# Optimization experiments

Hardware: AMD Instinct MI355X
Metric: run time of the kernel (lower is better)

Reference implementation:

```python
import jax, jax.numpy as jnp
import numpy as np

B, G = 32, 100                      # batch, max ground-truth boxes per image
LEVELS = [(80, 8), (40, 16), (20, 32)]  # (grid_size, stride) for 640x640 input -> 8400 anchors
NUM_CLASSES = 1


def _grids():
    xs, ys, ss = [], [], []
    for n, s in LEVELS:
        yy, xx = np.meshgrid(np.arange(n), np.arange(n), indexing="ij")
        xs.append(xx.reshape(-1)); ys.append(yy.reshape(-1)); ss.append(np.full(n * n, s))
    f = lambda a: jnp.asarray(np.concatenate(a), jnp.float32)[None]
    return f(xs), f(ys), f(ss)


def setup_inputs() -> dict:
    key = jax.random.key(0)
    k1, k2, k3, k4, k5, k6 = jax.random.split(key, 6)
    x_shifts, y_shifts, strides = _grids()
    A = x_shifts.shape[1]
    # decoded predictions: cx,cy in image, positive w,h; obj/cls are raw logits
    cxy = jax.random.uniform(k1, (B, A, 2), minval=0.0, maxval=640.0)
    wh = jax.random.uniform(k2, (B, A, 2), minval=4.0, maxval=128.0)
    objcls = jax.random.normal(k3, (B, A, 1 + NUM_CLASSES))
    outputs = jnp.concatenate([cxy, wh, objcls], -1)
    # labels: (class, cx, cy, w, h), zero-padded past the per-image gt count
    gxy = jax.random.uniform(k4, (B, G, 2), minval=32.0, maxval=608.0)
    gwh = jax.random.uniform(k5, (B, G, 2), minval=8.0, maxval=128.0)
    ngt = jax.random.randint(k6, (B,), 1, G + 1)
    valid = (jnp.arange(G)[None, :] < ngt[:, None]).astype(jnp.float32)[..., None]
    labels = jnp.concatenate([jnp.zeros((B, G, 1)), gxy, gwh], -1) * valid
    return {"outputs": outputs, "labels": labels, "x_shifts": x_shifts,
            "y_shifts": y_shifts, "expanded_strides": strides}


def _pairwise_iou_cxcywh(a, b):  # a [G,4] gt, b [A,4] preds -> [G,A]
    tl = jnp.maximum(a[:, None, :2] - a[:, None, 2:] / 2, b[None, :, :2] - b[None, :, 2:] / 2)
    br = jnp.minimum(a[:, None, :2] + a[:, None, 2:] / 2, b[None, :, :2] + b[None, :, 2:] / 2)
    inter = jnp.prod(jnp.maximum(br - tl, 0.0), -1)
    area_a = jnp.prod(a[:, 2:], -1)[:, None]
    area_b = jnp.prod(b[:, 2:], -1)[None, :]
    return inter / (area_a + area_b - inter + 1e-12)


def _assign_one(out, lab, xc, yc, st):
    """SimOTA assignment for one image. out [A,6], lab [G,5], xc/yc/st [A]."""
    bbox, obj, cls = out[:, :4], out[:, 4:5], out[:, 5:]
    valid_gt = lab.sum(-1) > 0                       # [G] mirrors nlabel logic
    gt = lab[:, 1:5]
    gt_cls = lab[:, 0].astype(jnp.int32)
    gcx, gcy, gw, gh = gt[:, 0:1], gt[:, 1:2], gt[:, 2:3], gt[:, 3:4]
    # anchor center inside gt box
    in_box = ((xc[None] > gcx - gw / 2) & (xc[None] < gcx + gw / 2) &
              (yc[None] > gcy - gh / 2) & (yc[None] < gcy + gh / 2))
    # anchor center within 2.5*stride of gt center
    r = 2.5 * st[None]
    in_ctr = (jnp.abs(xc[None] - gcx) < r) & (jnp.abs(yc[None] - gcy) < r)
    in_box &= valid_gt[:, None]
    in_ctr &= valid_gt[:, None]
    fg = (in_box | in_ctr).any(0)                    # [A] candidate fg anchors
    geo = in_box & in_ctr                            # [G,A]
    pair_ok = fg[None, :] & valid_gt[:, None]
    ious = _pairwise_iou_cxcywh(gt, bbox)            # [G,A]
    iou_m = jnp.where(pair_ok, ious, 0.0)
    # cls cost: BCE( sqrt(sigmoid(cls)*sigmoid(obj)), one_hot(gt_cls) )
    p = jnp.sqrt(jax.nn.sigmoid(cls) * jax.nn.sigmoid(obj))      # [A,C]
    t = jax.nn.one_hot(gt_cls, NUM_CLASSES)                       # [G,C]
    cls_cost = -(t[:, None, :] * jnp.log(p[None] + 1e-9) +
                 (1.0 - t[:, None, :]) * jnp.log(1.0 - p[None] + 1e-9)).sum(-1)
    cost = cls_cost + 3.0 * (-jnp.log(ious + 1e-8)) + 1e5 * (~geo)
    cost = jnp.where(pair_ok, cost, 1e9)             # exclude non-fg / padded gts
    # dynamic-k: k_g = clamp(sum(top-10 ious), min 1)
    topk_ious = jax.lax.top_k(iou_m, 10)[0]
    dyn_k = jnp.maximum(topk_ious.sum(-1).astype(jnp.int32), 1)  # [G]
    # rank anchors per gt by ascending cost; pick rank < dyn_k
    ranks = jnp.argsort(jnp.argsort(cost, axis=1), axis=1)
    matching = (ranks < dyn_k[:, None]) & pair_ok
    # resolve anchors matched to >1 gt: keep the min-cost gt
    cnt = matching.sum(0)
    best_gt = jnp.argmin(cost, 0)                    # [A]
    matching = jnp.where((cnt > 1)[None, :], jnp.arange(G)[:, None] == best_gt[None, :], matching)
    fg_final = matching.any(0)                       # [A]
    pred_iou = (matching.astype(ious.dtype) * ious).sum(0)       # [A]
    matched_gt = jnp.argmax(matching, 0)             # [A]
    cls_t = jax.nn.one_hot(gt_cls[matched_gt], NUM_CLASSES) * pred_iou[:, None]
    cls_t = jnp.where(fg_final[:, None], cls_t, 0.0)
    return fg_final, cls_t


def reference(outputs, labels, x_shifts, y_shifts, expanded_strides):
    st = expanded_strides[0]
    xc = (x_shifts[0] + 0.5) * st
    yc = (y_shifts[0] + 0.5) * st
    fg, cls_t = jax.vmap(lambda o, l: _assign_one(o, l, xc, yc, st))(outputs, labels)
    # assignment runs under no_grad in the original
    fg = jax.lax.stop_gradient(fg)
    cls_t = jax.lax.stop_gradient(cls_t)
    logits = outputs[:, :, 5:]                       # [B,A,C]
    bce = cls_t * jax.nn.softplus(-logits) + (1.0 - cls_t) * jax.nn.softplus(logits)
    num_fg = jnp.maximum(fg.sum().astype(jnp.float32), 1.0)
    return (bce * fg[..., None]).sum() / num_fg
```

## Files before the change

### kernel.cpp

```cpp
#include <hip/hip_runtime.h>
#include <hip/hip_bf16.h>
#include <stdint.h>

#define BB 32
#define GG 100
#define AA 8400
#define TPB 256
#define NCH 33
#define TKB 512
#define BA (BB*AA)
#define NG (BB*GG)
#define NB2 (BB*GG)
#define NITB 17
#define PCAP 8416
#define GCAP 128
#define SCAP (GG*10)

typedef __hip_bfloat16 bf16;

struct P {
  const void *outs, *labs, *ss;
  float4 *box4, *gtb, *gtc;
  float2 *aux2;
  float *pcc, *zl;
  int   *sel_a;
  float *sel_iou;
  int   *cnt, *own;
  float *pb, *pf;
  int *gmax;
  float *out;
};

__device__ __forceinline__ int dtypeFlag(const void* ss){
  return (((const uint32_t*)ss)[0] == 0x41000000u) ? 1 : 0;
}
__device__ __forceinline__ float ld(const void* p, int i, int isf32){
  return isf32 ? ((const float*)p)[i] : __bfloat162float(((const bf16*)p)[i]);
}
__device__ __forceinline__ void ageom(int a, float& xc, float& yc, float& r){
  int x, y, s;
  if (a < 6400){ x = a % 80; y = a / 80; s = 8; }
  else if (a < 8000){ int q = a - 6400; x = q % 40; y = q / 40; s = 16; }
  else { int q = a - 8000; x = q % 20; y = q / 20; s = 32; }
  float fs = (float)s;
  xc = ((float)x + 0.5f) * fs;
  yc = ((float)y + 0.5f) * fs;
  r  = 2.5f * fs;
}
__device__ __forceinline__ uint32_t apack2(int a){
  int x, y, s, lvl;
  if (a < 6400){ x = a % 80; y = a / 80; s = 8; lvl = 0; }
  else if (a < 8000){ int q = a - 6400; x = q % 40; y = q / 40; s = 16; lvl = 1; }
  else { int q = a - 8000; x = q % 20; y = q / 20; s = 32; lvl = 2; }
  return (uint32_t)(x*s + s/2) | ((uint32_t)(y*s + s/2) << 10) | ((uint32_t)lvl << 20);
}

__global__ __launch_bounds__(TPB) void kA(P p){
  __shared__ float4 s_gtb[GG], s_gtc[GG];
  __shared__ float s_o[TPB*6];
  __shared__ int s_ng;
  int t = threadIdx.x;
  int c = blockIdx.x, b = blockIdx.y;
  int isf = dtypeFlag(p.ss);
  if (t == 0) s_ng = 0;
  {
    int s = c*TPB + t;
    if (s < SCAP) p.sel_a[b*SCAP + s] = -1;
  }
  int nel = min(TPB*6, AA*6 - c*(TPB*6));
  if (isf){
    const float4* src = (const float4*)((const float*)p.outs + (size_t)b*AA*6 + (size_t)c*(TPB*6));
    float4* dst = (float4*)s_o;
    for (int i = t; i < nel/4; i += TPB) dst[i] = src[i];
  } else {
    const uint4* src = (const uint4*)((const bf16*)p.outs + (size_t)b*AA*6 + (size_t)c*(TPB*6));
    for (int i = t; i < nel/8; i += TPB){
      uint4 u = src[i];
      int o = i*8;
      s_o[o+0]=__uint_as_float(u.x<<16); s_o[o+1]=__uint_as_float(u.x&0xffff0000u);
      s_o[o+2]=__uint_as_float(u.y<<16); s_o[o+3]=__uint_as_float(u.y&0xffff0000u);
      s_o[o+4]=__uint_as_float(u.z<<16); s_o[o+5]=__uint_as_float(u.z&0xffff0000u);
      s_o[o+6]=__uint_as_float(u.w<<16); s_o[o+7]=__uint_as_float(u.w&0xffff0000u);
    }
  }
  __syncthreads();
  if (t < GG){
    int i = b*GG + t;
    float l0 = ld(p.labs, i*5  , isf);
    float gcx= ld(p.labs, i*5+1, isf);
    float gcy= ld(p.labs, i*5+2, isf);
    float gw = ld(p.labs, i*5+3, isf);
    float gh = ld(p.labs, i*5+4, isf);
    int valid = (l0+gcx+gcy+gw+gh) > 0.f;
    float4 vb = make_float4(gcx-gw*0.5f, gcy-gh*0.5f, gcx+gw*0.5f, gcy+gh*0.5f);
    float4 vc = make_float4(gcx, gcy, gw*gh, valid ? 1.f : 0.f);
    s_gtb[t] = vb; s_gtc[t] = vc;
    if (c == 0){ p.gtb[i] = vb; p.gtc[i] = vc; }
    if (valid) atomicMax(&s_ng, t+1);
  }
  __syncthreads();
  int ng = s_ng;
  if (c == 0 && t == 0) p.gmax[b] = ng;
  int a = c*TPB + t;
  if (a < AA){
    float cx=s_o[t*6], cy=s_o[t*6+1], w=s_o[t*6+2], h=s_o[t*6+3], ob=s_o[t*6+4], cl=s_o[t*6+5];
    int idx = b*AA + a;
    p.box4[idx] = make_float4(cx-w*0.5f, cy-h*0.5f, cx+w*0.5f, cy+h*0.5f);
    float so = 1.f/(1.f+expf(-ob));
    float sc = 1.f/(1.f+expf(-cl));
    float pccv = -logf(sqrtf(sc*so) + 1e-9f);
    float xc, yc, r; ageom(a, xc, yc, r);
    int fg = 0;
    for (int g = 0; g < ng; ++g){
      float4 gb = s_gtb[g], gc = s_gtc[g];
      bool inb = (xc>gb.x)&&(xc<gb.z)&&(yc>gb.y)&&(yc<gb.w);
      bool inc = (fabsf(xc-gc.x)<r)&&(fabsf(yc-gc.y)<r);
      fg |= (gc.w != 0.f) && (inb||inc);
    }
    float area = w*h;
    p.aux2[idx] = make_float2(fg ? area : -area, __uint_as_float(apack2(a)));
    p.pcc[idx] = pccv;
    p.zl [idx] = cl;
    p.cnt[idx] = 0;
    p.own[idx] = 0x7fffffff;
  }
}

__global__ __launch_bounds__(TKB) void kB(P p){
  __shared__ float s_pos[PCAP];
  __shared__ float s_gcost[GCAP];
  __shared__ int   s_gpos[GCAP];
  __shared__ int   s_pcnt, s_gcnt;
  int t = threadIdx.x;
  int lane = t & 63, wid = t >> 6;
  int item = blockIdx.x;
  int b = item / GG, g = item - b*GG;
  if (t == 0){ s_pcnt = 0; s_gcnt = 0; }
  float4 gc = p.gtc[b*GG+g];
  if (gc.w == 0.f) return;
  float4 gb = p.gtb[b*GG+g];
  float glx=gb.x, gly=gb.y, ghx=gb.z, ghy=gb.w, gcx=gc.x, gcy=gc.y, ga=gc.z;
  int base = b*AA;
  unsigned long long lmlt = (1ull<<lane) - 1ull;
  __syncthreads();

  for (int it = 0; it < NITB; ++it){
    int pos = it*TKB + t;
    bool ovl = false, geo = false;
    float v = 0.f, cst = 0.f;
    if (pos < AA){
      float2 aux = p.aux2[base+pos];
      float4 bx  = p.box4[base+pos];
      bool fg = aux.x > 0.f;
      uint32_t u = __float_as_uint(aux.y);
      float xc = (float)(u & 1023u), yc = (float)((u>>10)&1023u);
      float r  = (float)(20u << (u>>20));
      bool inb = (xc>glx)&&(xc<ghx)&&(yc>gly)&&(yc<ghy);
      geo = inb && (fabsf(xc-gcx)<r) && (fabsf(yc-gcy)<r);
      float tlx=fmaxf(glx,bx.x), tly=fmaxf(gly,bx.y);
      float brx=fminf(ghx,bx.z), bry=fminf(ghy,bx.w);
      float iw=brx-tlx, ih=bry-tly;
      ovl = fg && (iw>0.f) && (ih>0.f);
      if (ovl | geo){
        float area = fabsf(aux.x);
        float inter = fmaxf(iw,0.f)*fmaxf(ih,0.f);
        v = inter/(ga + area - inter + 1e-12f);
        if (geo) cst = p.pcc[base+pos] + 3.f*(-logf(v+1e-8f));
      }
    }
    unsigned long long m1 = __ballot(ovl);
    if (m1){
      int ldr = (int)(__ffsll(m1)-1);
      int off;
      if (lane == ldr) off = atomicAdd(&s_pcnt, __popcll(m1));
      off = __shfl(off, ldr);
      if (ovl) s_pos[off + __popcll(m1 & lmlt)] = v;
    }
    unsigned long long m2 = __ballot(geo);
    if (m2){
      int ldr = (int)(__ffsll(m2)-1);
      int off;
      if (lane == ldr) off = atomicAdd(&s_gcnt, __popcll(m2));
      off = __shfl(off, ldr);
      if (geo){
        int q = off + __popcll(m2 & lmlt);
        s_gcost[q] = cst; s_gpos[q] = pos;
      }
    }
  }
  __syncthreads();
  if (wid) return;

  int pcnt = s_pcnt, gcnt = s_gcnt;

  float lmax = -1.f;
  for (int i = lane; i < pcnt; i += 64) lmax = fmaxf(lmax, s_pos[i]);
  float sum = 0.f;
  for (int k = 0; k < 10; ++k){
    float gv = lmax;
#pragma unroll
    for (int off=32; off; off>>=1) gv = fmaxf(gv, __shfl_xor(gv, off));
    if (gv <= 0.f) break;
    sum += gv;
    unsigned long long ms = __ballot(lmax == gv);
    if ((int)(__ffsll(ms)-1) == lane){
      bool fnd = false; float nl = -1.f;
      for (int i = lane; i < pcnt; i += 64){
        float vv = s_pos[i];
        if (!fnd && vv == gv){ fnd = true; vv = -1.f; s_pos[i] = vv; }
        nl = fmaxf(nl, vv);
      }
      lmax = nl;
    }
  }
  int dk = (int)sum; if (dk<1) dk=1; if (dk>10) dk=10;

  float c0=3.0e38f, c1=3.0e38f; int p0=0x7fffffff, p1=0x7fffffff;
  if (lane < gcnt){ c0 = s_gcost[lane]; p0 = s_gpos[lane]; }
  if (lane+64 < gcnt){ c1 = s_gcost[lane+64]; p1 = s_gpos[lane+64]; }
  if (c1 < c0 || (c1==c0 && p1<p0)){
    float tc=c0; c0=c1; c1=tc; int tp=p0; p0=p1; p1=tp;
  }
  int mysel = -1, take = 0;
  for (int k = 0; k < dk; ++k){
    float gv=c0; int gi=p0;
#pragma unroll
    for (int off=32; off; off>>=1){
      float ov=__shfl_xor(gv,off); int oi=__shfl_xor(gi,off);
      if (ov<gv || (ov==gv && oi<gi)){ gv=ov; gi=oi; }
    }
    if (gv >= 2.9e38f) break;
    if (lane == k) mysel = gi;
    take++;
    if (c0==gv && p0==gi){ c0=c1; p0=p1; c1=3.0e38f; p1=0x7fffffff; }
  }

  float lastc = -3.0e38f; int lastp = -1;
  for (int k = take; k < dk; ++k){
    float bc = 3.0e38f; int bp = 0x7fffffff;
    int n64 = (AA + 63) >> 6;
    for (int it = 0; it < n64; ++it){
      int pos = (it<<6) + lane;
      if (pos < AA){
        float2 aux = p.aux2[base+pos];
        bool fg = aux.x > 0.f;
        if (fg){
          uint32_t u = __float_as_uint(aux.y);
          float xc = (float)(u & 1023u), yc = (float)((u>>10)&1023u);
          float r  = (float)(20u << (u>>20));
          bool inb = (xc>glx)&&(xc<ghx)&&(yc>gly)&&(yc<ghy);
          bool geo2 = inb && (fabsf(xc-gcx)<r) && (fabsf(yc-gcy)<r);
          if (!geo2){
            float4 bx = p.box4[base+pos];
            float tlx=fmaxf(glx,bx.x), tly=fmaxf(gly,bx.y);
            float brx=fminf(ghx,bx.z), bry=fminf(ghy,bx.w);
            float iw=fmaxf(brx-tlx,0.f), ih=fmaxf(bry-tly,0.f);
            float inter=iw*ih;
            float area = fabsf(aux.x);
            float v = inter/(ga + area - inter + 1e-12f);
            float cst = p.pcc[base+pos] + 3.f*(-logf(v+1e-8f)) + 100000.f;
            bool gt = (cst > lastc) || (cst == lastc && pos > lastp);
            bool lt = (cst < bc)   || (cst == bc   && pos < bp);
            if (gt && lt){ bc = cst; bp = pos; }
          }
        }
      }
    }
#pragma unroll
    for (int off=32; off; off>>=1){
      float ov=__shfl_xor(bc,off); int oi=__shfl_xor(bp,off);
      if (ov<bc || (ov==bc && oi<bp)){ bc=ov; bp=oi; }
    }
    if (bc >= 2.9e38f) break;
    if (lane == k) mysel = bp;
    lastc = bc; lastp = bp;
  }

  if (mysel >= 0){
    int a = mysel;
    float4 bx = p.box4[base+a];
    float area = fabsf(p.aux2[base+a].x);
    float tlx=fmaxf(glx,bx.x), tly=fmaxf(gly,bx.y);
    float brx=fminf(ghx,bx.z), bry=fminf(ghy,bx.w);
    float iw=fmaxf(brx-tlx,0.f), ih=fmaxf(bry-tly,0.f);
    float inter=iw*ih;
    float iou=inter/(ga + area - inter + 1e-12f);
    int slot = g*10 + lane;
    p.sel_a [b*SCAP + slot] = a;
    p.sel_iou[b*SCAP + slot] = iou;
    atomicAdd(&p.cnt[base+a], 1);
    atomicMin(&p.own[base+a], slot);
  }
}

__global__ __launch_bounds__(64) void kR(P p){
  int lane = threadIdx.x;
  int item = blockIdx.x;
  int b = item / GG, g = item - b*GG;
  int base = b*AA;
  int a = -1, cgt = 0;
  bool ownr = false;
  float iouv = 0.f;
  if (lane < 10){
    int slot = g*10 + lane;
    a = p.sel_a[b*SCAP + slot];
    if (a >= 0 && p.own[base+a] == slot){
      ownr = true;
      cgt = p.cnt[base+a];
      iouv = p.sel_iou[b*SCAP + slot];
    }
  }
  unsigned long long cm = __ballot(ownr && cgt > 1);
  if (cm){
    int ng = p.gmax[b];
    while (cm){
      int s = (int)(__ffsll(cm)-1); cm &= cm - 1ull;
      int aa = __shfl(a, s);
      float area = fabsf(p.aux2[base+aa].x);
      float pccv = p.pcc[base+aa];
      float4 bx = p.box4[base+aa];
      float xc,yc,r; ageom(aa,xc,yc,r);
      float bc = 3.9e38f, bi = 0.f; int bg = 0x7fffffff;
      for (int g2 = lane; g2 < ng; g2 += 64){
        float4 gbb = p.gtb[b*GG+g2], gcc = p.gtc[b*GG+g2];
        float cost, iou2 = 0.f;
        if (gcc.w != 0.f){
          float tlx=fmaxf(gbb.x,bx.x), tly=fmaxf(gbb.y,bx.y);
          float brx=fminf(gbb.z,bx.z), bry=fminf(gbb.w,bx.w);
          float iw=fmaxf(brx-tlx,0.f), ih=fmaxf(bry-tly,0.f);
          float inter=iw*ih;
          iou2 = inter/(gcc.z + area - inter + 1e-12f);
          bool inb=(xc>gbb.x)&&(xc<gbb.z)&&(yc>gbb.y)&&(yc<gbb.w);
          bool inc=(fabsf(xc-gcc.x)<r)&&(fabsf(yc-gcc.y)<r);
          cost = pccv + 3.f*(-logf(iou2+1e-8f)) + ((inb&&inc)?0.f:100000.f);
        } else cost = 1e9f;
        if (cost < bc){ bc=cost; bi=iou2; bg=g2; }
      }
#pragma unroll
      for (int off=32; off; off>>=1){
        float oc=__shfl_xor(bc,off), oi=__shfl_xor(bi,off);
        int og=__shfl_xor(bg,off);
        if (oc<bc || (oc==bc && og<bg)){ bc=oc; bi=oi; bg=og; }
      }
      if (lane == s) iouv = bi;
    }
  }
  float bce = 0.f, fgv = 0.f;
  if (lane < 10 && ownr){
    float z = p.zl[base+a];
    float e = expf(-fabsf(z));
    float spz = fmaxf(z,0.f)+log1pf(e);
    float spn = fmaxf(-z,0.f)+log1pf(e);
    bce = iouv*spn + (1.f-iouv)*spz;
    fgv = 1.f;
  }
#pragma unroll
  for (int off=32; off; off>>=1){
    bce += __shfl_xor(bce, off);
    fgv += __shfl_xor(fgv, off);
  }
  if (lane == 0){ p.pb[item] = bce; p.pf[item] = fgv; }
}

__global__ __launch_bounds__(TPB) void kD(P p){
  int t = threadIdx.x;
  float sb=0.f, sf=0.f;
  for (int i = t; i < NB2; i += TPB){ sb += p.pb[i]; sf += p.pf[i]; }
#pragma unroll
  for (int off=32; off; off>>=1){
    sb += __shfl_xor(sb, off);
    sf += __shfl_xor(sf, off);
  }
  __shared__ float s_b[4], s_f[4];
  int lane = t & 63, wid = t >> 6;
  if (lane==0){ s_b[wid]=sb; s_f[wid]=sf; }
  __syncthreads();
  if (t==0){
    float tb=s_b[0]+s_b[1]+s_b[2]+s_b[3];
    float tf=s_f[0]+s_f[1]+s_f[2]+s_f[3];
    p.out[0] = tb / fmaxf(tf, 1.f);
  }
}

extern "C" void kernel_launch(void* const* d_in, const int* in_sizes, int n_in,
                              void* d_out, int out_size, void* d_ws, size_t ws_size,
                              hipStream_t stream) {
  P p;
  p.outs = d_in[0];
  p.labs = d_in[1];
  p.ss   = d_in[4];
  char* w = (char*)d_ws;
  p.box4  = (float4*)w; w += (size_t)BA*sizeof(float4);
  p.gtb   = (float4*)w; w += (size_t)NG*sizeof(float4);
  p.gtc   = (float4*)w; w += (size_t)NG*sizeof(float4);
  p.aux2  = (float2*)w; w += (size_t)BA*sizeof(float2);
  p.pcc   = (float*)w;  w += (size_t)BA*sizeof(float);
  p.zl    = (float*)w;  w += (size_t)BA*sizeof(float);
  p.sel_a = (int*)w;    w += (size_t)BB*SCAP*sizeof(int);
  p.sel_iou=(float*)w;  w += (size_t)BB*SCAP*sizeof(float);
  p.cnt   = (int*)w;    w += (size_t)BA*sizeof(int);
  p.own   = (int*)w;    w += (size_t)BA*sizeof(int);
  p.gmax  = (int*)w;    w += (size_t)BB*sizeof(int);
  p.pb    = (float*)w;  w += (size_t)NB2*sizeof(float);
  p.pf    = (float*)w;  w += (size_t)NB2*sizeof(float);
  p.out   = (float*)d_out;

  kA<<<dim3(NCH, BB), TPB, 0, stream>>>(p);
  kB<<<BB*GG, TKB, 0, stream>>>(p);
  kR<<<NB2, 64, 0, stream>>>(p);
  kD<<<1, TPB, 0, stream>>>(p);
}
```

Before: 151.3 us.

## Drop precomputed per-anchor buffers; pack anchor metadata and read raw outputs

kA no longer writes box4, aux2, pcc and zl per anchor. It writes only a packed 32-bit word holding anchor geometry plus the fg flag, and the per-anchor count and owner are merged into one int2. kB and kR now read the raw prediction rows directly and recompute box corners, area and pair cost on the fly. The fg loop also exits early once a match is found. This is meant to cut workspace write and read traffic, at the cost of repeated transcendental work and strided 24-byte row reads in the per-GT blocks.

```diff
diff --git a/kernel.cpp b/kernel.cpp
--- a/kernel.cpp
+++ b/kernel.cpp
@@ -20,12 +20,11 @@
 
 struct P {
   const void *outs, *labs, *ss;
-  float4 *box4, *gtb, *gtc;
-  float2 *aux2;
-  float *pcc, *zl;
+  float4 *gtb, *gtc;
+  uint32_t *pk;
+  int2  *cnow;
   int   *sel_a;
   float *sel_iou;
-  int   *cnt, *own;
   float *pb, *pf;
   int *gmax;
   float *out;
@@ -36,6 +35,36 @@
 }
 __device__ __forceinline__ float ld(const void* p, int i, int isf32){
   return isf32 ? ((const float*)p)[i] : __bfloat162float(((const bf16*)p)[i]);
+}
+__device__ __forceinline__ void ldbox(const void* outs, int isf, size_t row,
+                                      float& cx, float& cy, float& w, float& h){
+  if (isf){
+    const float2* rw = (const float2*)((const float*)outs + row*6);
+    float2 r01 = rw[0], r23 = rw[1];
+    cx=r01.x; cy=r01.y; w=r23.x; h=r23.y;
+  } else {
+    const uint32_t* rw = (const uint32_t*)((const bf16*)outs + row*6);
+    uint32_t w0 = rw[0], w1 = rw[1];
+    cx=__uint_as_float(w0<<16); cy=__uint_as_float(w0&0xffff0000u);
+    w =__uint_as_float(w1<<16); h =__uint_as_float(w1&0xffff0000u);
+  }
+}
+__device__ __forceinline__ void ldoc(const void* outs, int isf, size_t row,
+                                     float& ob, float& cl){
+  if (isf){
+    const float2* rw = (const float2*)((const float*)outs + row*6);
+    float2 r45 = rw[2];
+    ob=r45.x; cl=r45.y;
+  } else {
+    const uint32_t* rw = (const uint32_t*)((const bf16*)outs + row*6);
+    uint32_t w2 = rw[2];
+    ob=__uint_as_float(w2<<16); cl=__uint_as_float(w2&0xffff0000u);
+  }
+}
+__device__ __forceinline__ float pccf(float ob, float cl){
+  float so = 1.f/(1.f+expf(-ob));
+  float sc = 1.f/(1.f+expf(-cl));
+  return -logf(sqrtf(sc*so) + 1e-9f);
 }
 __device__ __forceinline__ void ageom(int a, float& xc, float& yc, float& r){
   int x, y, s;
@@ -57,7 +86,6 @@
 
 __global__ __launch_bounds__(TPB) void kA(P p){
   __shared__ float4 s_gtb[GG], s_gtc[GG];
-  __shared__ float s_o[TPB*6];
   __shared__ int s_ng;
   int t = threadIdx.x;
   int c = blockIdx.x, b = blockIdx.y;
@@ -66,22 +94,6 @@
   {
     int s = c*TPB + t;
     if (s < SCAP) p.sel_a[b*SCAP + s] = -1;
-  }
-  int nel = min(TPB*6, AA*6 - c*(TPB*6));
-  if (isf){
-    const float4* src = (const float4*)((const float*)p.outs + (size_t)b*AA*6 + (size_t)c*(TPB*6));
-    float4* dst = (float4*)s_o;
-    for (int i = t; i < nel/4; i += TPB) dst[i] = src[i];
-  } else {
-    const uint4* src = (const uint4*)((const bf16*)p.outs + (size_t)b*AA*6 + (size_t)c*(TPB*6));
-    for (int i = t; i < nel/8; i += TPB){
-      uint4 u = src[i];
-      int o = i*8;
-      s_o[o+0]=__uint_as_float(u.x<<16); s_o[o+1]=__uint_as_float(u.x&0xffff0000u);
-      s_o[o+2]=__uint_as_float(u.y<<16); s_o[o+3]=__uint_as_float(u.y&0xffff0000u);
-      s_o[o+4]=__uint_as_float(u.z<<16); s_o[o+5]=__uint_as_float(u.z&0xffff0000u);
-      s_o[o+6]=__uint_as_float(u.w<<16); s_o[o+7]=__uint_as_float(u.w&0xffff0000u);
-    }
   }
   __syncthreads();
   if (t < GG){
@@ -103,12 +115,7 @@
   if (c == 0 && t == 0) p.gmax[b] = ng;
   int a = c*TPB + t;
   if (a < AA){
-    float cx=s_o[t*6], cy=s_o[t*6+1], w=s_o[t*6+2], h=s_o[t*6+3], ob=s_o[t*6+4], cl=s_o[t*6+5];
     int idx = b*AA + a;
-    p.box4[idx] = make_float4(cx-w*0.5f, cy-h*0.5f, cx+w*0.5f, cy+h*0.5f);
-    float so = 1.f/(1.f+expf(-ob));
-    float sc = 1.f/(1.f+expf(-cl));
-    float pccv = -logf(sqrtf(sc*so) + 1e-9f);
     float xc, yc, r; ageom(a, xc, yc, r);
     int fg = 0;
     for (int g = 0; g < ng; ++g){
@@ -116,13 +123,10 @@
       bool inb = (xc>gb.x)&&(xc<gb.z)&&(yc>gb.y)&&(yc<gb.w);
       bool inc = (fabsf(xc-gc.x)<r)&&(fabsf(yc-gc.y)<r);
       fg |= (gc.w != 0.f) && (inb||inc);
-    }
-    float area = w*h;
-    p.aux2[idx] = make_float2(fg ? area : -area, __uint_as_float(apack2(a)));
-    p.pcc[idx] = pccv;
-    p.zl [idx] = cl;
-    p.cnt[idx] = 0;
-    p.own[idx] = 0x7fffffff;
+      if (fg) break;
+    }
+    p.pk[idx]   = apack2(a) | (fg ? 0x80000000u : 0u);
+    p.cnow[idx] = make_int2(0, 0x7fffffff);
   }
 }
 
@@ -141,6 +145,7 @@
   float4 gb = p.gtb[b*GG+g];
   float glx=gb.x, gly=gb.y, ghx=gb.z, ghy=gb.w, gcx=gc.x, gcy=gc.y, ga=gc.z;
   int base = b*AA;
+  int isf = dtypeFlag(p.ss);
   unsigned long long lmlt = (1ull<<lane) - 1ull;
   __syncthreads();
 
@@ -149,23 +154,26 @@
     bool ovl = false, geo = false;
     float v = 0.f, cst = 0.f;
     if (pos < AA){
-      float2 aux = p.aux2[base+pos];
-      float4 bx  = p.box4[base+pos];
-      bool fg = aux.x > 0.f;
-      uint32_t u = __float_as_uint(aux.y);
+      uint32_t u = p.pk[base+pos];
+      bool fg = (u & 0x80000000u) != 0;
       float xc = (float)(u & 1023u), yc = (float)((u>>10)&1023u);
-      float r  = (float)(20u << (u>>20));
+      float r  = (float)(20u << ((u>>20)&3u));
       bool inb = (xc>glx)&&(xc<ghx)&&(yc>gly)&&(yc<ghy);
       geo = inb && (fabsf(xc-gcx)<r) && (fabsf(yc-gcy)<r);
-      float tlx=fmaxf(glx,bx.x), tly=fmaxf(gly,bx.y);
-      float brx=fminf(ghx,bx.z), bry=fminf(ghy,bx.w);
+      float cx,cy,w,h; ldbox(p.outs, isf, (size_t)(base+pos), cx,cy,w,h);
+      float blx=cx-w*0.5f, bly=cy-h*0.5f, bhx=cx+w*0.5f, bhy=cy+h*0.5f;
+      float tlx=fmaxf(glx,blx), tly=fmaxf(gly,bly);
+      float brx=fminf(ghx,bhx), bry=fminf(ghy,bhy);
       float iw=brx-tlx, ih=bry-tly;
       ovl = fg && (iw>0.f) && (ih>0.f);
       if (ovl | geo){
-        float area = fabsf(aux.x);
+        float area = w*h;
         float inter = fmaxf(iw,0.f)*fmaxf(ih,0.f);
         v = inter/(ga + area - inter + 1e-12f);
-        if (geo) cst = p.pcc[base+pos] + 3.f*(-logf(v+1e-8f));
+        if (geo){
+          float ob,cl; ldoc(p.outs, isf, (size_t)(base+pos), ob, cl);
+          cst = pccf(ob,cl) + 3.f*(-logf(v+1e-8f));
+        }
       }
     }
     unsigned long long m1 = __ballot(ovl);
@@ -242,23 +250,24 @@
     for (int it = 0; it < n64; ++it){
       int pos = (it<<6) + lane;
       if (pos < AA){
-        float2 aux = p.aux2[base+pos];
-        bool fg = aux.x > 0.f;
+        uint32_t u = p.pk[base+pos];
+        bool fg = (u & 0x80000000u) != 0;
         if (fg){
-          uint32_t u = __float_as_uint(aux.y);
           float xc = (float)(u & 1023u), yc = (float)((u>>10)&1023u);
-          float r  = (float)(20u << (u>>20));
+          float r  = (float)(20u << ((u>>20)&3u));
           bool inb = (xc>glx)&&(xc<ghx)&&(yc>gly)&&(yc<ghy);
           bool geo2 = inb && (fabsf(xc-gcx)<r) && (fabsf(yc-gcy)<r);
           if (!geo2){
-            float4 bx = p.box4[base+pos];
-            float tlx=fmaxf(glx,bx.x), tly=fmaxf(gly,bx.y);
-            float brx=fminf(ghx,bx.z), bry=fminf(ghy,bx.w);
+            float cx,cy,w,h; ldbox(p.outs, isf, (size_t)(base+pos), cx,cy,w,h);
+            float blx=cx-w*0.5f, bly=cy-h*0.5f, bhx=cx+w*0.5f, bhy=cy+h*0.5f;
+            float tlx=fmaxf(glx,blx), tly=fmaxf(gly,bly);
+            float brx=fminf(ghx,bhx), bry=fminf(ghy,bhy);
             float iw=fmaxf(brx-tlx,0.f), ih=fmaxf(bry-tly,0.f);
             float inter=iw*ih;
-            float area = fabsf(aux.x);
+            float area = w*h;
             float v = inter/(ga + area - inter + 1e-12f);
-            float cst = p.pcc[base+pos] + 3.f*(-logf(v+1e-8f)) + 100000.f;
+            float ob,cl; ldoc(p.outs, isf, (size_t)(base+pos), ob, cl);
+            float cst = pccf(ob,cl) + 3.f*(-logf(v+1e-8f)) + 100000.f;
             bool gt = (cst > lastc) || (cst == lastc && pos > lastp);
             bool lt = (cst < bc)   || (cst == bc   && pos < bp);
             if (gt && lt){ bc = cst; bp = pos; }
@@ -278,18 +287,19 @@
 
   if (mysel >= 0){
     int a = mysel;
-    float4 bx = p.box4[base+a];
-    float area = fabsf(p.aux2[base+a].x);
-    float tlx=fmaxf(glx,bx.x), tly=fmaxf(gly,bx.y);
-    float brx=fminf(ghx,bx.z), bry=fminf(ghy,bx.w);
+    float cx,cy,w,h; ldbox(p.outs, isf, (size_t)(base+a), cx,cy,w,h);
+    float blx=cx-w*0.5f, bly=cy-h*0.5f, bhx=cx+w*0.5f, bhy=cy+h*0.5f;
+    float area = w*h;
+    float tlx=fmaxf(glx,blx), tly=fmaxf(gly,bly);
+    float brx=fminf(ghx,bhx), bry=fminf(ghy,bhy);
     float iw=fmaxf(brx-tlx,0.f), ih=fmaxf(bry-tly,0.f);
     float inter=iw*ih;
     float iou=inter/(ga + area - inter + 1e-12f);
     int slot = g*10 + lane;
     p.sel_a [b*SCAP + slot] = a;
     p.sel_iou[b*SCAP + slot] = iou;
-    atomicAdd(&p.cnt[base+a], 1);
-    atomicMin(&p.own[base+a], slot);
+    atomicAdd(&p.cnow[base+a].x, 1);
+    atomicMin(&p.cnow[base+a].y, slot);
   }
 }
 
@@ -298,16 +308,20 @@
   int item = blockIdx.x;
   int b = item / GG, g = item - b*GG;
   int base = b*AA;
+  int isf = dtypeFlag(p.ss);
   int a = -1, cgt = 0;
   bool ownr = false;
   float iouv = 0.f;
   if (lane < 10){
     int slot = g*10 + lane;
     a = p.sel_a[b*SCAP + slot];
-    if (a >= 0 && p.own[base+a] == slot){
-      ownr = true;
-      cgt = p.cnt[base+a];
-      iouv = p.sel_iou[b*SCAP + slot];
+    if (a >= 0){
+      int2 co = p.cnow[base+a];
+      if (co.y == slot){
+        ownr = true;
+        cgt = co.x;
+        iouv = p.sel_iou[b*SCAP + slot];
+      }
     }
   }
   unsigned long long cm = __ballot(ownr && cgt > 1);
@@ -316,17 +330,19 @@
     while (cm){
       int s = (int)(__ffsll(cm)-1); cm &= cm - 1ull;
       int aa = __shfl(a, s);
-      float area = fabsf(p.aux2[base+aa].x);
-      float pccv = p.pcc[base+aa];
-      float4 bx = p.box4[base+aa];
+      float cx,cy,w,h; ldbox(p.outs, isf, (size_t)(base+aa), cx,cy,w,h);
+      float ob,cl; ldoc(p.outs, isf, (size_t)(base+aa), ob, cl);
+      float area = w*h;
+      float pccv = pccf(ob,cl);
+      float blx=cx-w*0.5f, bly=cy-h*0.5f, bhx=cx+w*0.5f, bhy=cy+h*0.5f;
       float xc,yc,r; ageom(aa,xc,yc,r);
       float bc = 3.9e38f, bi = 0.f; int bg = 0x7fffffff;
       for (int g2 = lane; g2 < ng; g2 += 64){
         float4 gbb = p.gtb[b*GG+g2], gcc = p.gtc[b*GG+g2];
         float cost, iou2 = 0.f;
         if (gcc.w != 0.f){
-          float tlx=fmaxf(gbb.x,bx.x), tly=fmaxf(gbb.y,bx.y);
-          float brx=fminf(gbb.z,bx.z), bry=fminf(gbb.w,bx.w);
+          float tlx=fmaxf(gbb.x,blx), tly=fmaxf(gbb.y,bly);
+          float brx=fminf(gbb.z,bhx), bry=fminf(gbb.w,bhy);
           float iw=fmaxf(brx-tlx,0.f), ih=fmaxf(bry-tly,0.f);
           float inter=iw*ih;
           iou2 = inter/(gcc.z + area - inter + 1e-12f);
@@ -347,7 +363,8 @@
   }
   float bce = 0.f, fgv = 0.f;
   if (lane < 10 && ownr){
-    float z = p.zl[base+a];
+    float ob,cl; ldoc(p.outs, isf, (size_t)(base+a), ob, cl);
+    float z = cl;
     float e = expf(-fabsf(z));
     float spz = fmaxf(z,0.f)+log1pf(e);
     float spn = fmaxf(-z,0.f)+log1pf(e);
@@ -390,16 +407,12 @@
   p.labs = d_in[1];
   p.ss   = d_in[4];
   char* w = (char*)d_ws;
-  p.box4  = (float4*)w; w += (size_t)BA*sizeof(float4);
   p.gtb   = (float4*)w; w += (size_t)NG*sizeof(float4);
   p.gtc   = (float4*)w; w += (size_t)NG*sizeof(float4);
-  p.aux2  = (float2*)w; w += (size_t)BA*sizeof(float2);
-  p.pcc   = (float*)w;  w += (size_t)BA*sizeof(float);
-  p.zl    = (float*)w;  w += (size_t)BA*sizeof(float);
+  p.pk    = (uint32_t*)w; w += (size_t)BA*sizeof(uint32_t);
+  p.cnow  = (int2*)w;   w += (size_t)BA*sizeof(int2);
   p.sel_a = (int*)w;    w += (size_t)BB*SCAP*sizeof(int);
   p.sel_iou=(float*)w;  w += (size_t)BB*SCAP*sizeof(float);
-  p.cnt   = (int*)w;    w += (size_t)BA*sizeof(int);
-  p.own   = (int*)w;    w += (size_t)BA*sizeof(int);
   p.gmax  = (int*)w;    w += (size_t)BB*sizeof(int);
   p.pb    = (float*)w;  w += (size_t)NB2*sizeof(float);
   p.pf    = (float*)w;  w += (size_t)NB2*sizeof(float);
```

Measured after the change: 159.7 us. +5.5%, slower.

## Split per-GT candidate scan into anchor-chunked partial top-10 and merge kernels

Applied to the files above, without the earlier changes.

Replaces the per-(image,GT) kernel that scanned all 8400 anchors with a kernel tiled over anchor chunks. It keeps each chunk's anchor data in registers and loops over GTs across waves, writing a partial top-10 IoU list per chunk plus global geometric-candidate lists. A new small merge kernel then reduces the 33 partial top-10 lists per GT and reads the candidate costs. This aims to cut redundant anchor reloads and the large shared buffer, at the cost of an extra launch, global atomics, and workspace traffic. It also adds an early break in kA's foreground check.

```diff
diff --git a/kernel.cpp b/kernel.cpp
--- a/kernel.cpp
+++ b/kernel.cpp
@@ -7,14 +7,12 @@
 #define AA 8400
 #define TPB 256
 #define NCH 33
-#define TKB 512
 #define BA (BB*AA)
 #define NG (BB*GG)
 #define NB2 (BB*GG)
-#define NITB 17
-#define PCAP 8416
 #define GCAP 128
 #define SCAP (GG*10)
+#define NT10 (NCH*10)
 
 typedef __hip_bfloat16 bf16;
 
@@ -23,6 +21,10 @@
   float4 *box4, *gtb, *gtc;
   float2 *aux2;
   float *pcc, *zl;
+  float *top10;
+  float *gcostL;
+  int   *gposL;
+  int   *gct;
   int   *sel_a;
   float *sel_iou;
   int   *cnt, *own;
@@ -66,6 +68,7 @@
   {
     int s = c*TPB + t;
     if (s < SCAP) p.sel_a[b*SCAP + s] = -1;
+    if (s < GG)   p.gct[b*GG + s] = 0;
   }
   int nel = min(TPB*6, AA*6 - c*(TPB*6));
   if (isf){
@@ -116,6 +119,7 @@
       bool inb = (xc>gb.x)&&(xc<gb.z)&&(yc>gb.y)&&(yc<gb.w);
       bool inc = (fabsf(xc-gc.x)<r)&&(fabsf(yc-gc.y)<r);
       fg |= (gc.w != 0.f) && (inb||inc);
+      if (fg) break;
     }
     float area = w*h;
     p.aux2[idx] = make_float2(fg ? area : -area, __uint_as_float(apack2(a)));
@@ -126,75 +130,110 @@
   }
 }
 
-__global__ __launch_bounds__(TKB) void kB(P p){
-  __shared__ float s_pos[PCAP];
-  __shared__ float s_gcost[GCAP];
-  __shared__ int   s_gpos[GCAP];
-  __shared__ int   s_pcnt, s_gcnt;
+__global__ __launch_bounds__(TPB) void kS(P p){
+  __shared__ float4 s_gtb[GG], s_gtc[GG];
   int t = threadIdx.x;
+  int c = blockIdx.x, b = blockIdx.y;
   int lane = t & 63, wid = t >> 6;
-  int item = blockIdx.x;
-  int b = item / GG, g = item - b*GG;
-  if (t == 0){ s_pcnt = 0; s_gcnt = 0; }
-  float4 gc = p.gtc[b*GG+g];
-  if (gc.w == 0.f) return;
-  float4 gb = p.gtb[b*GG+g];
-  float glx=gb.x, gly=gb.y, ghx=gb.z, ghy=gb.w, gcx=gc.x, gcy=gc.y, ga=gc.z;
+  if (t < GG){ s_gtb[t] = p.gtb[b*GG+t]; s_gtc[t] = p.gtc[b*GG+t]; }
+  __syncthreads();
+  int ng = p.gmax[b];
   int base = b*AA;
+  int a0 = c*TPB;
+  float2 ax[4]; float4 bxr[4];
+#pragma unroll
+  for (int q=0;q<4;q++){
+    int a = a0 + q*64 + lane;
+    if (a < AA){ ax[q] = p.aux2[base+a]; bxr[q] = p.box4[base+a]; }
+    else { ax[q] = make_float2(-1.f, 0.f); bxr[q] = make_float4(0,0,0,0); }
+  }
   unsigned long long lmlt = (1ull<<lane) - 1ull;
-  __syncthreads();
-
-  for (int it = 0; it < NITB; ++it){
-    int pos = it*TKB + t;
-    bool ovl = false, geo = false;
-    float v = 0.f, cst = 0.f;
-    if (pos < AA){
-      float2 aux = p.aux2[base+pos];
-      float4 bx  = p.box4[base+pos];
+
+  for (int g = wid; g < ng; g += 4){
+    float4 gc = s_gtc[g];
+    if (gc.w == 0.f) continue;
+    float4 gb = s_gtb[g];
+    float glx=gb.x, gly=gb.y, ghx=gb.z, ghy=gb.w, gcx=gc.x, gcy=gc.y, ga=gc.z;
+    float v[4];
+#pragma unroll
+    for (int q=0;q<4;q++){
+      float2 aux = ax[q]; float4 bb = bxr[q];
       bool fg = aux.x > 0.f;
       uint32_t u = __float_as_uint(aux.y);
       float xc = (float)(u & 1023u), yc = (float)((u>>10)&1023u);
       float r  = (float)(20u << (u>>20));
       bool inb = (xc>glx)&&(xc<ghx)&&(yc>gly)&&(yc<ghy);
-      geo = inb && (fabsf(xc-gcx)<r) && (fabsf(yc-gcy)<r);
-      float tlx=fmaxf(glx,bx.x), tly=fmaxf(gly,bx.y);
-      float brx=fminf(ghx,bx.z), bry=fminf(ghy,bx.w);
+      bool geo = inb && (fabsf(xc-gcx)<r) && (fabsf(yc-gcy)<r);
+      float tlx=fmaxf(glx,bb.x), tly=fmaxf(gly,bb.y);
+      float brx=fminf(ghx,bb.z), bry=fminf(ghy,bb.w);
       float iw=brx-tlx, ih=bry-tly;
-      ovl = fg && (iw>0.f) && (ih>0.f);
+      bool ovl = fg && (iw>0.f) && (ih>0.f);
+      float vv = 0.f;
       if (ovl | geo){
         float area = fabsf(aux.x);
         float inter = fmaxf(iw,0.f)*fmaxf(ih,0.f);
-        v = inter/(ga + area - inter + 1e-12f);
-        if (geo) cst = p.pcc[base+pos] + 3.f*(-logf(v+1e-8f));
-      }
-    }
-    unsigned long long m1 = __ballot(ovl);
-    if (m1){
-      int ldr = (int)(__ffsll(m1)-1);
-      int off;
-      if (lane == ldr) off = atomicAdd(&s_pcnt, __popcll(m1));
-      off = __shfl(off, ldr);
-      if (ovl) s_pos[off + __popcll(m1 & lmlt)] = v;
-    }
-    unsigned long long m2 = __ballot(geo);
-    if (m2){
-      int ldr = (int)(__ffsll(m2)-1);
-      int off;
-      if (lane == ldr) off = atomicAdd(&s_gcnt, __popcll(m2));
-      off = __shfl(off, ldr);
-      if (geo){
-        int q = off + __popcll(m2 & lmlt);
-        s_gcost[q] = cst; s_gpos[q] = pos;
-      }
-    }
-  }
-  __syncthreads();
-  if (wid) return;
-
-  int pcnt = s_pcnt, gcnt = s_gcnt;
-
-  float lmax = -1.f;
-  for (int i = lane; i < pcnt; i += 64) lmax = fmaxf(lmax, s_pos[i]);
+        vv = inter/(ga + area - inter + 1e-12f);
+      }
+      v[q] = ovl ? vv : 0.f;
+      unsigned long long m2 = __ballot(geo);
+      if (m2){
+        int ldr = (int)(__ffsll(m2)-1);
+        int off;
+        if (lane == ldr) off = atomicAdd(&p.gct[b*GG+g], __popcll(m2));
+        off = __shfl(off, ldr);
+        if (geo){
+          int a = a0 + q*64 + lane;
+          float cst = p.pcc[base+a] + 3.f*(-logf(vv+1e-8f));
+          int qq = off + __popcll(m2 & lmlt);
+          p.gcostL[(size_t)(b*GG+g)*GCAP + qq] = cst;
+          p.gposL [(size_t)(b*GG+g)*GCAP + qq] = a;
+        }
+      }
+    }
+    float* dst = &p.top10[((size_t)(b*GG+g)*NCH + c)*10];
+    float lmax = fmaxf(fmaxf(v[0],v[1]), fmaxf(v[2],v[3]));
+    int k = 0;
+    for (; k < 10; ++k){
+      float gv = lmax;
+#pragma unroll
+      for (int off=32; off; off>>=1) gv = fmaxf(gv, __shfl_xor(gv, off));
+      if (gv <= 0.f) break;
+      if (lane == 0) dst[k] = gv;
+      unsigned long long ms = __ballot(lmax == gv);
+      if ((int)(__ffsll(ms)-1) == lane){
+        bool fnd = false; float nl = 0.f;
+#pragma unroll
+        for (int q=0;q<4;q++){
+          float vv = v[q];
+          if (!fnd && vv == gv){ fnd = true; vv = 0.f; v[q] = vv; }
+          nl = fmaxf(nl, vv);
+        }
+        lmax = nl;
+      }
+    }
+    if (lane == 0) for (int kk=k; kk<10; ++kk) dst[kk] = 0.f;
+  }
+}
+
+__global__ __launch_bounds__(64) void kM(P p){
+  int lane = threadIdx.x;
+  int item = blockIdx.x;
+  int b = item / GG, g = item - b*GG;
+  float4 gc = p.gtc[item];
+  if (gc.w == 0.f) return;
+  float4 gb = p.gtb[item];
+  float glx=gb.x, gly=gb.y, ghx=gb.z, ghy=gb.w, gcx=gc.x, gcy=gc.y, ga=gc.z;
+  int base = b*AA;
+
+  float r6[6];
+#pragma unroll
+  for (int q=0;q<6;q++){
+    int i = q*64 + lane;
+    r6[q] = (i < NT10) ? p.top10[(size_t)item*NT10 + i] : 0.f;
+  }
+  float lmax = 0.f;
+#pragma unroll
+  for (int q=0;q<6;q++) lmax = fmaxf(lmax, r6[q]);
   float sum = 0.f;
   for (int k = 0; k < 10; ++k){
     float gv = lmax;
@@ -204,10 +243,11 @@
     sum += gv;
     unsigned long long ms = __ballot(lmax == gv);
     if ((int)(__ffsll(ms)-1) == lane){
-      bool fnd = false; float nl = -1.f;
-      for (int i = lane; i < pcnt; i += 64){
-        float vv = s_pos[i];
-        if (!fnd && vv == gv){ fnd = true; vv = -1.f; s_pos[i] = vv; }
+      bool fnd = false; float nl = 0.f;
+#pragma unroll
+      for (int q=0;q<6;q++){
+        float vv = r6[q];
+        if (!fnd && vv == gv){ fnd = true; vv = 0.f; r6[q] = vv; }
         nl = fmaxf(nl, vv);
       }
       lmax = nl;
@@ -215,9 +255,10 @@
   }
   int dk = (int)sum; if (dk<1) dk=1; if (dk>10) dk=10;
 
+  int gcnt = p.gct[item];
   float c0=3.0e38f, c1=3.0e38f; int p0=0x7fffffff, p1=0x7fffffff;
-  if (lane < gcnt){ c0 = s_gcost[lane]; p0 = s_gpos[lane]; }
-  if (lane+64 < gcnt){ c1 = s_gcost[lane+64]; p1 = s_gpos[lane+64]; }
+  if (lane < gcnt){ c0 = p.gcostL[(size_t)item*GCAP+lane]; p0 = p.gposL[(size_t)item*GCAP+lane]; }
+  if (lane+64 < gcnt){ c1 = p.gcostL[(size_t)item*GCAP+lane+64]; p1 = p.gposL[(size_t)item*GCAP+lane+64]; }
   if (c1 < c0 || (c1==c0 && p1<p0)){
     float tc=c0; c0=c1; c1=tc; int tp=p0; p0=p1; p1=tp;
   }
@@ -396,6 +437,10 @@
   p.aux2  = (float2*)w; w += (size_t)BA*sizeof(float2);
   p.pcc   = (float*)w;  w += (size_t)BA*sizeof(float);
   p.zl    = (float*)w;  w += (size_t)BA*sizeof(float);
+  p.top10 = (float*)w;  w += (size_t)NB2*NT10*sizeof(float);
+  p.gcostL= (float*)w;  w += (size_t)NB2*GCAP*sizeof(float);
+  p.gposL = (int*)w;    w += (size_t)NB2*GCAP*sizeof(int);
+  p.gct   = (int*)w;    w += (size_t)NB2*sizeof(int);
   p.sel_a = (int*)w;    w += (size_t)BB*SCAP*sizeof(int);
   p.sel_iou=(float*)w;  w += (size_t)BB*SCAP*sizeof(float);
   p.cnt   = (int*)w;    w += (size_t)BA*sizeof(int);
@@ -406,7 +451,8 @@
   p.out   = (float*)d_out;
 
   kA<<<dim3(NCH, BB), TPB, 0, stream>>>(p);
-  kB<<<BB*GG, TKB, 0, stream>>>(p);
+  kS<<<dim3(NCH, BB), TPB, 0, stream>>>(p);
+  kM<<<NB2, 64, 0, stream>>>(p);
   kR<<<NB2, 64, 0, stream>>>(p);
   kD<<<1, TPB, 0, stream>>>(p);
 }
```

Result: slower. 230.7 us (+52.4%).

## Split per-GT anchor scan across four blocks and merge top-10 in new kernel

Applied to the files above, without the earlier changes.

The per-ground-truth kernel that scanned all 8400 anchors in one block is split into four blocks, each covering a quarter of the anchors. Each block writes its partial top-10 IoUs and appends candidate costs to global lists through a global atomic counter. A new small merge kernel combines the partial top-10s, computes dynamic k, and continues the cost selection. The intent is more parallelism and smaller shared memory per block so more blocks fit per CU, at the cost of an extra launch, global atomics and extra global traffic. The anchor prefilter loop also exits early once a match is found.

```diff
diff --git a/kernel.cpp b/kernel.cpp
--- a/kernel.cpp
+++ b/kernel.cpp
@@ -8,13 +8,16 @@
 #define TPB 256
 #define NCH 33
 #define TKB 512
+#define NSP 4
+#define SPAN (AA/NSP)
+#define NITS 5
 #define BA (BB*AA)
 #define NG (BB*GG)
 #define NB2 (BB*GG)
-#define NITB 17
-#define PCAP 8416
+#define SCAP2 2112
 #define GCAP 128
 #define SCAP (GG*10)
+#define NT10 (NSP*10)
 
 typedef __hip_bfloat16 bf16;
 
@@ -23,6 +26,10 @@
   float4 *box4, *gtb, *gtc;
   float2 *aux2;
   float *pcc, *zl;
+  float *top10;
+  float *gcostL;
+  int   *gposL;
+  int   *gct;
   int   *sel_a;
   float *sel_iou;
   int   *cnt, *own;
@@ -66,6 +73,7 @@
   {
     int s = c*TPB + t;
     if (s < SCAP) p.sel_a[b*SCAP + s] = -1;
+    if (s < GG)   p.gct[b*GG + s] = 0;
   }
   int nel = min(TPB*6, AA*6 - c*(TPB*6));
   if (isf){
@@ -116,6 +124,7 @@
       bool inb = (xc>gb.x)&&(xc<gb.z)&&(yc>gb.y)&&(yc<gb.w);
       bool inc = (fabsf(xc-gc.x)<r)&&(fabsf(yc-gc.y)<r);
       fg |= (gc.w != 0.f) && (inb||inc);
+      if (fg) break;
     }
     float area = w*h;
     p.aux2[idx] = make_float2(fg ? area : -area, __uint_as_float(apack2(a)));
@@ -126,29 +135,29 @@
   }
 }
 
-__global__ __launch_bounds__(TKB) void kB(P p){
-  __shared__ float s_pos[PCAP];
-  __shared__ float s_gcost[GCAP];
-  __shared__ int   s_gpos[GCAP];
-  __shared__ int   s_pcnt, s_gcnt;
+__global__ __launch_bounds__(TKB) void kSp(P p){
+  __shared__ float s_pos[SCAP2];
+  __shared__ int   s_pcnt;
   int t = threadIdx.x;
   int lane = t & 63, wid = t >> 6;
-  int item = blockIdx.x;
+  int bid = blockIdx.x;
+  int item = bid >> 2, h = bid & 3;
   int b = item / GG, g = item - b*GG;
-  if (t == 0){ s_pcnt = 0; s_gcnt = 0; }
-  float4 gc = p.gtc[b*GG+g];
+  if (t == 0) s_pcnt = 0;
+  float4 gc = p.gtc[item];
   if (gc.w == 0.f) return;
-  float4 gb = p.gtb[b*GG+g];
+  float4 gb = p.gtb[item];
   float glx=gb.x, gly=gb.y, ghx=gb.z, ghy=gb.w, gcx=gc.x, gcy=gc.y, ga=gc.z;
   int base = b*AA;
+  int lo = h*SPAN, hi = lo + SPAN;
   unsigned long long lmlt = (1ull<<lane) - 1ull;
   __syncthreads();
 
-  for (int it = 0; it < NITB; ++it){
-    int pos = it*TKB + t;
+  for (int it = 0; it < NITS; ++it){
+    int pos = lo + it*TKB + t;
     bool ovl = false, geo = false;
     float v = 0.f, cst = 0.f;
-    if (pos < AA){
+    if (pos < hi){
       float2 aux = p.aux2[base+pos];
       float4 bx  = p.box4[base+pos];
       bool fg = aux.x > 0.f;
@@ -180,28 +189,29 @@
     if (m2){
       int ldr = (int)(__ffsll(m2)-1);
       int off;
-      if (lane == ldr) off = atomicAdd(&s_gcnt, __popcll(m2));
+      if (lane == ldr) off = atomicAdd(&p.gct[item], __popcll(m2));
       off = __shfl(off, ldr);
       if (geo){
         int q = off + __popcll(m2 & lmlt);
-        s_gcost[q] = cst; s_gpos[q] = pos;
+        p.gcostL[(size_t)item*GCAP + q] = cst;
+        p.gposL [(size_t)item*GCAP + q] = pos;
       }
     }
   }
   __syncthreads();
   if (wid) return;
 
-  int pcnt = s_pcnt, gcnt = s_gcnt;
-
+  int pcnt = s_pcnt;
+  float* dst = &p.top10[(size_t)item*NT10 + h*10];
   float lmax = -1.f;
   for (int i = lane; i < pcnt; i += 64) lmax = fmaxf(lmax, s_pos[i]);
-  float sum = 0.f;
-  for (int k = 0; k < 10; ++k){
+  int k = 0;
+  for (; k < 10; ++k){
     float gv = lmax;
 #pragma unroll
     for (int off=32; off; off>>=1) gv = fmaxf(gv, __shfl_xor(gv, off));
     if (gv <= 0.f) break;
-    sum += gv;
+    if (lane == 0) dst[k] = gv;
     unsigned long long ms = __ballot(lmax == gv);
     if ((int)(__ffsll(ms)-1) == lane){
       bool fnd = false; float nl = -1.f;
@@ -213,11 +223,36 @@
       lmax = nl;
     }
   }
+  if (lane == 0) for (int kk=k; kk<10; ++kk) dst[kk] = 0.f;
+}
+
+__global__ __launch_bounds__(64) void kM(P p){
+  int lane = threadIdx.x;
+  int item = blockIdx.x;
+  int b = item / GG, g = item - b*GG;
+  float4 gc = p.gtc[item];
+  if (gc.w == 0.f) return;
+  float4 gb = p.gtb[item];
+  float glx=gb.x, gly=gb.y, ghx=gb.z, ghy=gb.w, gcx=gc.x, gcy=gc.y, ga=gc.z;
+  int base = b*AA;
+
+  float r0 = (lane < NT10) ? p.top10[(size_t)item*NT10 + lane] : 0.f;
+  float sum = 0.f;
+  for (int k = 0; k < 10; ++k){
+    float gv = r0;
+#pragma unroll
+    for (int off=32; off; off>>=1) gv = fmaxf(gv, __shfl_xor(gv, off));
+    if (gv <= 0.f) break;
+    sum += gv;
+    unsigned long long ms = __ballot(r0 == gv);
+    if ((int)(__ffsll(ms)-1) == lane) r0 = 0.f;
+  }
   int dk = (int)sum; if (dk<1) dk=1; if (dk>10) dk=10;
 
+  int gcnt = p.gct[item];
   float c0=3.0e38f, c1=3.0e38f; int p0=0x7fffffff, p1=0x7fffffff;
-  if (lane < gcnt){ c0 = s_gcost[lane]; p0 = s_gpos[lane]; }
-  if (lane+64 < gcnt){ c1 = s_gcost[lane+64]; p1 = s_gpos[lane+64]; }
+  if (lane < gcnt){ c0 = p.gcostL[(size_t)item*GCAP+lane]; p0 = p.gposL[(size_t)item*GCAP+lane]; }
+  if (lane+64 < gcnt){ c1 = p.gcostL[(size_t)item*GCAP+lane+64]; p1 = p.gposL[(size_t)item*GCAP+lane+64]; }
   if (c1 < c0 || (c1==c0 && p1<p0)){
     float tc=c0; c0=c1; c1=tc; int tp=p0; p0=p1; p1=tp;
   }
@@ -396,6 +431,10 @@
   p.aux2  = (float2*)w; w += (size_t)BA*sizeof(float2);
   p.pcc   = (float*)w;  w += (size_t)BA*sizeof(float);
   p.zl    = (float*)w;  w += (size_t)BA*sizeof(float);
+  p.top10 = (float*)w;  w += (size_t)NB2*NT10*sizeof(float);
+  p.gcostL= (float*)w;  w += (size_t)NB2*GCAP*sizeof(float);
+  p.gposL = (int*)w;    w += (size_t)NB2*GCAP*sizeof(int);
+  p.gct   = (int*)w;    w += (size_t)NB2*sizeof(int);
   p.sel_a = (int*)w;    w += (size_t)BB*SCAP*sizeof(int);
   p.sel_iou=(float*)w;  w += (size_t)BB*SCAP*sizeof(float);
   p.cnt   = (int*)w;    w += (size_t)BA*sizeof(int);
@@ -406,7 +445,8 @@
   p.out   = (float*)d_out;
 
   kA<<<dim3(NCH, BB), TPB, 0, stream>>>(p);
-  kB<<<BB*GG, TKB, 0, stream>>>(p);
+  kSp<<<NB2*NSP, TKB, 0, stream>>>(p);
+  kM<<<NB2, 64, 0, stream>>>(p);
   kR<<<NB2, 64, 0, stream>>>(p);
   kD<<<1, TPB, 0, stream>>>(p);
 }
```

Measured after the change: 165.9 us. 9.6% more time.
